# Kernel optimization log

Measured on AMD Instinct MI355X. Metric: run time of the kernel, lower is better.

## Reference

```python
import jax, jax.numpy as jnp
from jax import lax
import numpy as np

Bn, DM, HH, WW = 2, 192, 64, 64   # batch, d_model, H, W (H==W required by transpose-stack)
DI = 384   # d_inner = ssm_ratio * d_model
DS = 16    # ssm_d_state
ND = 4     # n_directions
CG = 12    # c_group
LN_EPS = 1e-5


def setup_inputs() -> dict:
    key = jax.random.key(0)
    k = jax.random.split(key, 16)
    w = lambda i, shape: jax.random.normal(k[i], shape, jnp.float32) * 0.05
    return {
        "x": jax.random.normal(k[0], (Bn, DM, HH, WW), jnp.float32),
        "in_proj_w": w(1, (DI, DM)),
        "dwconv_w": w(2, (DI, 1, 3, 3)),
        "dwconv_b": w(3, (DI,)),
        "x_down_w": w(4, (DS, DI)),
        "w_up_w": w(5, (CG * DI, DS)),
        "l_up_w": w(6, (ND * DI, DS)),
        "u_up_w": w(7, (ND * DI, DS)),
        "d_up_w": w(8, (ND * DI, DS)),
        "m_w": w(9, (ND,)),
        "grn_gamma": w(10, (DI,)),
        "grn_beta": w(11, (DI,)),
        "norm_w": 1.0 + w(12, (DI,)),
        "norm_b": w(13, (DI,)),
        "out_proj_w": w(14, (DM, DI)),
    }


def _conv1x1(w, x):
    return jnp.einsum('oc,bchw->bohw', w, x)


def _gate_recurrent(X, B, G1, G2, G3):
    # H[:, :, h, w] = B*X + G1*H[h-1,w-1] + G2*H[h,w-1] + G3*H[h+1,w-1]
    # sequential over width; vectorized over batch/channel/height via a column scan.
    def step(hprev, col):  # hprev: [B, C, H]
        xw, bw, g1w, g2w, g3w = col
        z = jnp.zeros_like(hprev[:, :, :1])
        up = jnp.concatenate([z, hprev[:, :, :-1]], axis=2)   # H[h-1, w-1]
        dn = jnp.concatenate([hprev[:, :, 1:], z], axis=2)    # H[h+1, w-1]
        h = bw * xw + g1w * up + g2w * hprev + g3w * dn
        return h, h

    cols = tuple(jnp.moveaxis(t, 3, 0) for t in (X, B, G1, G2, G3))  # [W, B, C, H]
    h0 = jnp.zeros(X.shape[:3], X.dtype)
    _, ys = lax.scan(step, h0, cols)
    return jnp.moveaxis(ys, 0, 3)  # [B, C, H, W]


def _normalize_w(Gl, Gm, Gr):
    gl, gm, gr = jax.nn.sigmoid(Gl), jax.nn.sigmoid(Gm), jax.nn.sigmoid(Gr)
    s = gl + gm + gr
    s = s.at[:, :, 0, :].set(gm[:, :, 0, :] + gr[:, :, 0, :])
    s = s.at[:, :, -1, :].set(gl[:, :, -1, :] + gm[:, :, -1, :])
    s = jnp.maximum(s, 1e-7)
    return gl / s, gm / s, gr / s


def reference(x, in_proj_w, dwconv_w, dwconv_b, x_down_w, w_up_w, l_up_w, u_up_w,
              d_up_w, m_w, grn_gamma, grn_beta, norm_w, norm_b, out_proj_w):
    Bsz = x.shape[0]
    # in_proj (1x1, no bias) + SiLU + depthwise 3x3 conv
    h = jax.nn.silu(_conv1x1(in_proj_w, x))
    h = lax.conv_general_dilated(h, dwconv_w, (1, 1), ((1, 1), (1, 1)),
                                 feature_group_count=DI) + dwconv_b[None, :, None, None]
    # forward_corev1
    xp = _conv1x1(x_down_w, h)            # [B, DS, H, W]
    ws = _conv1x1(w_up_w, xp)             # [B, 12*DI, H, W]
    Ls = _conv1x1(l_up_w, xp)             # [B, 4*DI, H, W]
    Us = _conv1x1(u_up_w, xp)
    Ds = _conv1x1(d_up_w, xp)
    hT = jnp.swapaxes(h, 2, 3)            # requires H==W
    xs = jnp.concatenate([h, hT, h[..., ::-1], hT[..., ::-1]], axis=1)  # [B, 4*DI, H, W]
    G1, G2, G3 = jnp.split(ws, 3, axis=1)
    g1, g2, g3 = _normalize_w(G1, G2, G3)
    out = _gate_recurrent(xs, Ls, g1, g2, g3)
    out = out * Us + xs * Ds
    # merge directions: view [B, 4, DI*H, W], 1x1 conv 4->1
    out = out.reshape(Bsz, ND, DI * HH, WW)
    y = jnp.einsum('d,bdxw->bxw', m_w, out).reshape(Bsz, DI, HH, WW)
    # LayerNorm2d over channel dim
    mu = y.mean(axis=1, keepdims=True)
    var = ((y - mu) ** 2).mean(axis=1, keepdims=True)
    y = (y - mu) * lax.rsqrt(var + LN_EPS) * norm_w[None, :, None, None] + norm_b[None, :, None, None]
    # GRN
    Gx = jnp.sqrt(jnp.sum(y * y, axis=(2, 3), keepdims=True))        # [B, C, 1, 1]
    Nx = Gx / (Gx.mean(axis=1, keepdims=True) + 1e-6)
    y = grn_gamma[None, :, None, None] * (y * Nx) + grn_beta[None, :, None, None] + y
    # out_proj (1x1, no bias)
    return _conv1x1(out_proj_w, y)
```

## Files before the change

### kernel.cpp

```cpp
#include <hip/hip_runtime.h>
#include <math.h>

#define Bn 2
#define DM 192
#define DI 384
#define DS 16
#define HH 64
#define WW 64
#define HW 4096
#define ND 4

__device__ __forceinline__ float sigmoidf_(float x) {
    return 1.0f / (1.0f + __expf(-x));
}

__global__ __launch_bounds__(256) void k_inproj(const float* __restrict__ x,
                                                const float* __restrict__ w,
                                                float* __restrict__ hpre) {
    int og = blockIdx.y, b = blockIdx.z;
    int p = blockIdx.x * 256 + threadIdx.x;
    const float* wr = w + (size_t)og * 16 * DM;
    const float* xb = x + (size_t)b * DM * HW + p;
    float acc[16];
#pragma unroll
    for (int j = 0; j < 16; ++j) acc[j] = 0.f;
    for (int c = 0; c < DM; c += 4) {
        float x0 = xb[(size_t)(c + 0) * HW];
        float x1 = xb[(size_t)(c + 1) * HW];
        float x2 = xb[(size_t)(c + 2) * HW];
        float x3 = xb[(size_t)(c + 3) * HW];
#pragma unroll
        for (int j = 0; j < 16; ++j) {
            const float* wj = wr + j * DM + c;
            acc[j] = fmaf(wj[0], x0, fmaf(wj[1], x1, fmaf(wj[2], x2, fmaf(wj[3], x3, acc[j]))));
        }
    }
    float* hb = hpre + (size_t)b * DI * HW + (size_t)(og * 16) * HW + p;
#pragma unroll
    for (int j = 0; j < 16; ++j) {
        float v = acc[j];
        hb[(size_t)j * HW] = v * (1.0f / (1.0f + __expf(-v)));
    }
}

__global__ __launch_bounds__(256) void k_dwconv(const float* __restrict__ hpre,
                                                const float* __restrict__ w,
                                                const float* __restrict__ bias,
                                                float* __restrict__ h) {
    int c = blockIdx.y, b = blockIdx.z;
    int p = blockIdx.x * 256 + threadIdx.x;
    int i = p >> 6, j = p & 63;
    const float* wp = w + c * 9;
    const float* src = hpre + ((size_t)b * DI + c) * HW;
    float acc = bias[c];
#pragma unroll
    for (int di = -1; di <= 1; ++di) {
        int ii = i + di;
        if (ii < 0 || ii >= HH) continue;
#pragma unroll
        for (int dj = -1; dj <= 1; ++dj) {
            int jj = j + dj;
            if (jj < 0 || jj >= WW) continue;
            acc = fmaf(wp[(di + 1) * 3 + (dj + 1)], src[ii * WW + jj], acc);
        }
    }
    h[((size_t)b * DI + c) * HW + p] = acc;
}

__global__ __launch_bounds__(256) void k_xdown(const float* __restrict__ h,
                                               const float* __restrict__ w,
                                               float* __restrict__ xpt) {
    int sq = blockIdx.y;
    int t = blockIdx.x * 256 + threadIdx.x;
    int b = t >> 12, p = t & 4095;
    const float* hb = h + (size_t)b * DI * HW + p;
    const float* w0 = w + (size_t)(4 * sq + 0) * DI;
    const float* w1 = w + (size_t)(4 * sq + 1) * DI;
    const float* w2 = w + (size_t)(4 * sq + 2) * DI;
    const float* w3 = w + (size_t)(4 * sq + 3) * DI;
    float a0 = 0.f, a1 = 0.f, a2 = 0.f, a3 = 0.f;
#pragma unroll 16
    for (int c = 0; c < DI; ++c) {
        float hv = hb[(size_t)c * HW];
        a0 = fmaf(w0[c], hv, a0);
        a1 = fmaf(w1[c], hv, a1);
        a2 = fmaf(w2[c], hv, a2);
        a3 = fmaf(w3[c], hv, a3);
    }
    float4 r = {a0, a1, a2, a3};
    *reinterpret_cast<float4*>(xpt + (size_t)t * 16 + 4 * sq) = r;
}

__global__ __launch_bounds__(256) void k_scan(const float* __restrict__ h,
                                              const float* __restrict__ xpt,
                                              const float* __restrict__ wup,
                                              const float* __restrict__ lup,
                                              const float* __restrict__ uup,
                                              const float* __restrict__ dup,
                                              const float* __restrict__ mw,
                                              float* __restrict__ y) {
    int c = blockIdx.x, b = blockIdx.y;
    int tid = threadIdx.x;
    int d = tid >> 6, hl = tid & 63;

    __shared__ float htile[64][65];
    __shared__ float acc[64][65];

    const float* hb = h + ((size_t)b * DI + c) * HW;
    for (int i = tid; i < HW; i += 256) {
        htile[i >> 6][i & 63] = hb[i];
        acc[i >> 6][i & 63] = 0.f;
    }

    int row = d * DI + c;
    const float* p1 = wup + (size_t)row * DS;
    const float* p2 = wup + (size_t)(4 * DI + row) * DS;
    const float* p3 = wup + (size_t)(8 * DI + row) * DS;
    const float* pL = lup + (size_t)row * DS;
    const float* pU = uup + (size_t)row * DS;
    const float* pD = dup + (size_t)row * DS;
    float w1[16], w2[16], w3[16], wL[16], wU[16], wD[16];
#pragma unroll
    for (int s = 0; s < 16; ++s) {
        w1[s] = p1[s]; w2[s] = p2[s]; w3[s] = p3[s];
        wL[s] = pL[s]; wU[s] = pU[s]; wD[s] = pD[s];
    }
    float md = mw[d];

    const float4* xq = reinterpret_cast<const float4*>(
        xpt + ((size_t)b * HW + (size_t)hl * 64) * DS);

    float4 c0 = xq[0], c1 = xq[1], c2 = xq[2], c3 = xq[3];
    float hprev = 0.f;
    __syncthreads();

    for (int w = 0; w < 64; ++w) {
        int nw = (w < 63) ? w + 1 : w;
        float4 n0 = xq[nw * 4 + 0], n1 = xq[nw * 4 + 1];
        float4 n2 = xq[nw * 4 + 2], n3 = xq[nw * 4 + 3];

        float xv[16] = {c0.x, c0.y, c0.z, c0.w, c1.x, c1.y, c1.z, c1.w,
                        c2.x, c2.y, c2.z, c2.w, c3.x, c3.y, c3.z, c3.w};
        float g1 = 0, g2 = 0, g3 = 0, L = 0, U = 0, Dv = 0;
#pragma unroll
        for (int s = 0; s < 16; ++s) {
            g1 = fmaf(w1[s], xv[s], g1);
            g2 = fmaf(w2[s], xv[s], g2);
            g3 = fmaf(w3[s], xv[s], g3);
            L  = fmaf(wL[s], xv[s], L);
            U  = fmaf(wU[s], xv[s], U);
            Dv = fmaf(wD[s], xv[s], Dv);
        }
        g1 = sigmoidf_(g1); g2 = sigmoidf_(g2); g3 = sigmoidf_(g3);
        float ssum = (hl == 0) ? (g2 + g3) : (hl == 63) ? (g1 + g2) : (g1 + g2 + g3);
        ssum = fmaxf(ssum, 1e-7f);
        float inv = 1.0f / ssum;
        float n1g = g1 * inv, n2g = g2 * inv, n3g = g3 * inv;

        float X;
        if (d == 0)      X = htile[hl][w];
        else if (d == 1) X = htile[w][hl];
        else if (d == 2) X = htile[hl][63 - w];
        else             X = htile[63 - w][hl];

        float up = __shfl_up(hprev, 1);
        float dn = __shfl_down(hprev, 1);
        if (hl == 0) up = 0.f;
        if (hl == 63) dn = 0.f;

        float hnew = fmaf(L, X, fmaf(n1g, up, fmaf(n2g, hprev, n3g * dn)));
        hprev = hnew;
        atomicAdd(&acc[hl][w], md * fmaf(hnew, U, X * Dv));

        c0 = n0; c1 = n1; c2 = n2; c3 = n3;
    }
    __syncthreads();
    float* yb = y + ((size_t)b * DI + c) * HW;
    for (int i = tid; i < HW; i += 256) yb[i] = acc[i >> 6][i & 63];
}

__global__ __launch_bounds__(256) void k_ln(float* __restrict__ y,
                                            const float* __restrict__ nw,
                                            const float* __restrict__ nb) {
    int lpx = threadIdx.x & 31, chunk = threadIdx.x >> 5;
    int gp = blockIdx.x * 32 + lpx;
    int b = gp >> 12, p = gp & 4095;
    float* yb = y + (size_t)b * DI * HW + p;

    float vv[48];
    float s = 0.f, s2 = 0.f;
#pragma unroll
    for (int ci = 0; ci < 48; ++ci) {
        float v = yb[(size_t)(chunk * 48 + ci) * HW];
        vv[ci] = v;
        s += v;
        s2 = fmaf(v, v, s2);
    }
    __shared__ float S[8][32], S2[8][32];
    S[chunk][lpx] = s;
    S2[chunk][lpx] = s2;
    __syncthreads();
    float ts = 0.f, ts2 = 0.f;
#pragma unroll
    for (int k = 0; k < 8; ++k) { ts += S[k][lpx]; ts2 += S2[k][lpx]; }
    float mu = ts * (1.0f / DI);
    float var = ts2 * (1.0f / DI) - mu * mu;
    float inv = rsqrtf(var + 1e-5f);
#pragma unroll
    for (int ci = 0; ci < 48; ++ci) {
        int c = chunk * 48 + ci;
        float v = (vv[ci] - mu) * inv;
        yb[(size_t)c * HW] = fmaf(v, nw[c], nb[c]);
    }
}

__global__ __launch_bounds__(256) void k_grnsum(const float* __restrict__ y,
                                                float* __restrict__ gx) {
    int c = blockIdx.x, b = blockIdx.y;
    const float* yb = y + ((size_t)b * DI + c) * HW;
    float s = 0.f;
#pragma unroll 4
    for (int i = threadIdx.x; i < HW; i += 256) {
        float v = yb[i];
        s = fmaf(v, v, s);
    }
#pragma unroll
    for (int o = 32; o > 0; o >>= 1) s += __shfl_down(s, o);
    __shared__ float red[4];
    int wid = threadIdx.x >> 6;
    if ((threadIdx.x & 63) == 0) red[wid] = s;
    __syncthreads();
    if (threadIdx.x == 0) gx[b * DI + c] = sqrtf(red[0] + red[1] + red[2] + red[3]);
}

__global__ __launch_bounds__(256) void k_grnscale(const float* __restrict__ gx,
                                                  const float* __restrict__ gamma,
                                                  float* __restrict__ sc) {
    int b = blockIdx.x;
    const float* g = gx + b * DI;
    float s = 0.f;
    for (int c = threadIdx.x; c < DI; c += 256) s += g[c];
#pragma unroll
    for (int o = 32; o > 0; o >>= 1) s += __shfl_down(s, o);
    __shared__ float red[4];
    __shared__ float meanv;
    int wid = threadIdx.x >> 6;
    if ((threadIdx.x & 63) == 0) red[wid] = s;
    __syncthreads();
    if (threadIdx.x == 0) meanv = (red[0] + red[1] + red[2] + red[3]) * (1.0f / DI);
    __syncthreads();
    float m = meanv;
    for (int c = threadIdx.x; c < DI; c += 256)
        sc[b * DI + c] = 1.0f + gamma[c] * (g[c] / (m + 1e-6f));
}

__global__ __launch_bounds__(256) void k_outproj(const float* __restrict__ y,
                                                 const float* __restrict__ w,
                                                 const float* __restrict__ sc_all,
                                                 const float* __restrict__ beta,
                                                 float* __restrict__ out) {
    int og = blockIdx.y, b = blockIdx.z;
    int p = blockIdx.x * 256 + threadIdx.x;
    const float* wr = w + (size_t)og * 8 * DI;
    const float* scb = sc_all + b * DI;
    const float* yb = y + (size_t)b * DI * HW + p;
    float acc[8];
#pragma unroll
    for (int j = 0; j < 8; ++j) acc[j] = 0.f;
    for (int c = 0; c < DI; c += 4) {
        float v0 = fmaf(yb[(size_t)(c + 0) * HW], scb[c + 0], beta[c + 0]);
        float v1 = fmaf(yb[(size_t)(c + 1) * HW], scb[c + 1], beta[c + 1]);
        float v2 = fmaf(yb[(size_t)(c + 2) * HW], scb[c + 2], beta[c + 2]);
        float v3 = fmaf(yb[(size_t)(c + 3) * HW], scb[c + 3], beta[c + 3]);
#pragma unroll
        for (int j = 0; j < 8; ++j) {
            const float* wj = wr + j * DI + c;
            acc[j] = fmaf(wj[0], v0, fmaf(wj[1], v1, fmaf(wj[2], v2, fmaf(wj[3], v3, acc[j]))));
        }
    }
    float* ob = out + (size_t)b * DM * HW + (size_t)(og * 8) * HW + p;
#pragma unroll
    for (int j = 0; j < 8; ++j) ob[(size_t)j * HW] = acc[j];
}

extern "C" void kernel_launch(void* const* d_in, const int* in_sizes, int n_in,
                              void* d_out, int out_size, void* d_ws, size_t ws_size,
                              hipStream_t stream) {
    (void)in_sizes; (void)n_in; (void)out_size; (void)ws_size;
    const float* x          = (const float*)d_in[0];
    const float* in_proj_w  = (const float*)d_in[1];
    const float* dwconv_w   = (const float*)d_in[2];
    const float* dwconv_b   = (const float*)d_in[3];
    const float* x_down_w   = (const float*)d_in[4];
    const float* w_up_w     = (const float*)d_in[5];
    const float* l_up_w     = (const float*)d_in[6];
    const float* u_up_w     = (const float*)d_in[7];
    const float* d_up_w     = (const float*)d_in[8];
    const float* m_w        = (const float*)d_in[9];
    const float* grn_gamma  = (const float*)d_in[10];
    const float* grn_beta   = (const float*)d_in[11];
    const float* norm_w     = (const float*)d_in[12];
    const float* norm_b     = (const float*)d_in[13];
    const float* out_proj_w = (const float*)d_in[14];

    float* ws = (float*)d_ws;
    const size_t NBIG = (size_t)Bn * DI * HW;
    float* hpre = ws;
    float* hbuf = ws + NBIG;
    float* xpt  = ws + 2 * NBIG;
    float* gx   = ws + 2 * NBIG + (size_t)Bn * HW * DS;
    float* sc   = gx + Bn * DI;
    float* y    = hpre;

    k_inproj<<<dim3(16, 24, 2), 256, 0, stream>>>(x, in_proj_w, hpre);
    k_dwconv<<<dim3(16, DI, Bn), 256, 0, stream>>>(hpre, dwconv_w, dwconv_b, hbuf);
    k_xdown<<<dim3(32, 4), 256, 0, stream>>>(hbuf, x_down_w, xpt);
    k_scan<<<dim3(DI, Bn), 256, 0, stream>>>(hbuf, xpt, w_up_w, l_up_w, u_up_w,
                                             d_up_w, m_w, y);
    k_ln<<<dim3(256), 256, 0, stream>>>(y, norm_w, norm_b);
    k_grnsum<<<dim3(DI, Bn), 256, 0, stream>>>(y, gx);
    k_grnscale<<<dim3(Bn), 256, 0, stream>>>(gx, grn_gamma, sc);
    k_outproj<<<dim3(16, 24, 2), 256, 0, stream>>>(y, out_proj_w, sc, grn_beta,
                                                   (float*)d_out);
}
```

Before: 227.2 us.

## Fuse GRN sum into LayerNorm, restructure xdown, streamline scan inner loop

The GRN sum-of-squares reduction moves into the LayerNorm kernel using wave shuffles and atomics, which removes a separate full pass over y. A memset is added to zero the accumulator. The x_down projection is rewritten so each block computes all 16 outputs for 64 pixels, splitting channels across waves and reducing through shared memory; this reads h once instead of four times. The scan loop precomputes the per-direction LDS pointer, folds m_w into the U/D weights, uses ds_bpermute and fast reciprocals, and double-buffers the xpt loads. Fast rcp slightly changes numerics, and the atomic float accumulation makes results order-dependent.

Result: slower. 289.8 us (+27.6%).

```diff
diff --git a/kernel.cpp b/kernel.cpp
--- a/kernel.cpp
+++ b/kernel.cpp
@@ -10,8 +10,9 @@
 #define HW 4096
 #define ND 4
 
-__device__ __forceinline__ float sigmoidf_(float x) {
-    return 1.0f / (1.0f + __expf(-x));
+__device__ __forceinline__ float fastrcp(float x) { return __builtin_amdgcn_rcpf(x); }
+__device__ __forceinline__ float fsig(float x) {
+    return fastrcp(1.0f + __expf(-x));
 }
 
 __global__ __launch_bounds__(256) void k_inproj(const float* __restrict__ x,
@@ -39,7 +40,7 @@
 #pragma unroll
     for (int j = 0; j < 16; ++j) {
         float v = acc[j];
-        hb[(size_t)j * HW] = v * (1.0f / (1.0f + __expf(-v)));
+        hb[(size_t)j * HW] = v * fastrcp(1.0f + __expf(-v));
     }
 }
 
@@ -70,25 +71,39 @@
 __global__ __launch_bounds__(256) void k_xdown(const float* __restrict__ h,
                                                const float* __restrict__ w,
                                                float* __restrict__ xpt) {
-    int sq = blockIdx.y;
-    int t = blockIdx.x * 256 + threadIdx.x;
-    int b = t >> 12, p = t & 4095;
+    __shared__ float red[4][64][17];
+    int tid = threadIdx.x;
+    int px = tid & 63, cw = tid >> 6;
+    int gp = blockIdx.x * 64 + px;
+    int b = gp >> 12, p = gp & 4095;
     const float* hb = h + (size_t)b * DI * HW + p;
-    const float* w0 = w + (size_t)(4 * sq + 0) * DI;
-    const float* w1 = w + (size_t)(4 * sq + 1) * DI;
-    const float* w2 = w + (size_t)(4 * sq + 2) * DI;
-    const float* w3 = w + (size_t)(4 * sq + 3) * DI;
-    float a0 = 0.f, a1 = 0.f, a2 = 0.f, a3 = 0.f;
-#pragma unroll 16
-    for (int c = 0; c < DI; ++c) {
-        float hv = hb[(size_t)c * HW];
-        a0 = fmaf(w0[c], hv, a0);
-        a1 = fmaf(w1[c], hv, a1);
-        a2 = fmaf(w2[c], hv, a2);
-        a3 = fmaf(w3[c], hv, a3);
-    }
-    float4 r = {a0, a1, a2, a3};
-    *reinterpret_cast<float4*>(xpt + (size_t)t * 16 + 4 * sq) = r;
+    int c0 = cw * 96;
+    float a[16];
+#pragma unroll
+    for (int s = 0; s < 16; ++s) a[s] = 0.f;
+    for (int cc = 0; cc < 96; cc += 4) {
+        float h0 = hb[(size_t)(c0 + cc + 0) * HW];
+        float h1 = hb[(size_t)(c0 + cc + 1) * HW];
+        float h2 = hb[(size_t)(c0 + cc + 2) * HW];
+        float h3 = hb[(size_t)(c0 + cc + 3) * HW];
+#pragma unroll
+        for (int s = 0; s < 16; ++s) {
+            const float* ws = w + (size_t)s * DI + c0 + cc;
+            a[s] = fmaf(ws[0], h0, fmaf(ws[1], h1, fmaf(ws[2], h2, fmaf(ws[3], h3, a[s]))));
+        }
+    }
+#pragma unroll
+    for (int s = 0; s < 16; ++s) red[cw][px][s] = a[s];
+    __syncthreads();
+    int sg = tid >> 6;
+    float4 r;
+    float* o = &r.x;
+#pragma unroll
+    for (int j = 0; j < 4; ++j) {
+        int s = sg * 4 + j;
+        o[j] = red[0][px][s] + red[1][px][s] + red[2][px][s] + red[3][px][s];
+    }
+    *reinterpret_cast<float4*>(xpt + (size_t)gp * 16 + sg * 4) = r;
 }
 
 __global__ __launch_bounds__(256) void k_scan(const float* __restrict__ h,
@@ -119,28 +134,38 @@
     const float* pL = lup + (size_t)row * DS;
     const float* pU = uup + (size_t)row * DS;
     const float* pD = dup + (size_t)row * DS;
+    float md = mw[d];
     float w1[16], w2[16], w3[16], wL[16], wU[16], wD[16];
 #pragma unroll
     for (int s = 0; s < 16; ++s) {
         w1[s] = p1[s]; w2[s] = p2[s]; w3[s] = p3[s];
-        wL[s] = pL[s]; wU[s] = pU[s]; wD[s] = pD[s];
-    }
-    float md = mw[d];
+        wL[s] = pL[s]; wU[s] = md * pU[s]; wD[s] = md * pD[s];
+    }
+
+    int xstep = (d & 1) ? 65 : 1;
+    int xbase = (d & 1) ? hl : hl * 65;
+    if (d & 2) { xbase += xstep * 63; xstep = -xstep; }
+    const float* xptr = &htile[0][0] + xbase;
+
+    int upA = ((hl - 1) & 63) << 2;
+    int dnA = ((hl + 1) & 63) << 2;
+    bool isTop = (hl == 0), isBot = (hl == 63);
+
+    float* accp = &acc[hl][0];
 
     const float4* xq = reinterpret_cast<const float4*>(
         xpt + ((size_t)b * HW + (size_t)hl * 64) * DS);
 
-    float4 c0 = xq[0], c1 = xq[1], c2 = xq[2], c3 = xq[3];
     float hprev = 0.f;
-    __syncthreads();
-
-    for (int w = 0; w < 64; ++w) {
-        int nw = (w < 63) ? w + 1 : w;
-        float4 n0 = xq[nw * 4 + 0], n1 = xq[nw * 4 + 1];
-        float4 n2 = xq[nw * 4 + 2], n3 = xq[nw * 4 + 3];
-
-        float xv[16] = {c0.x, c0.y, c0.z, c0.w, c1.x, c1.y, c1.z, c1.w,
-                        c2.x, c2.y, c2.z, c2.w, c3.x, c3.y, c3.z, c3.w};
+
+    float4 A0 = xq[0], A1 = xq[1], A2 = xq[2], A3 = xq[3];
+    float4 B0, B1, B2, B3;
+
+    __syncthreads();
+
+    auto docol = [&](const float4& q0, const float4& q1, const float4& q2, const float4& q3) {
+        float xv[16] = {q0.x, q0.y, q0.z, q0.w, q1.x, q1.y, q1.z, q1.w,
+                        q2.x, q2.y, q2.z, q2.w, q3.x, q3.y, q3.z, q3.w};
         float g1 = 0, g2 = 0, g3 = 0, L = 0, U = 0, Dv = 0;
 #pragma unroll
         for (int s = 0; s < 16; ++s) {
@@ -151,29 +176,30 @@
             U  = fmaf(wU[s], xv[s], U);
             Dv = fmaf(wD[s], xv[s], Dv);
         }
-        g1 = sigmoidf_(g1); g2 = sigmoidf_(g2); g3 = sigmoidf_(g3);
-        float ssum = (hl == 0) ? (g2 + g3) : (hl == 63) ? (g1 + g2) : (g1 + g2 + g3);
-        ssum = fmaxf(ssum, 1e-7f);
-        float inv = 1.0f / ssum;
-        float n1g = g1 * inv, n2g = g2 * inv, n3g = g3 * inv;
-
-        float X;
-        if (d == 0)      X = htile[hl][w];
-        else if (d == 1) X = htile[w][hl];
-        else if (d == 2) X = htile[hl][63 - w];
-        else             X = htile[63 - w][hl];
-
-        float up = __shfl_up(hprev, 1);
-        float dn = __shfl_down(hprev, 1);
-        if (hl == 0) up = 0.f;
-        if (hl == 63) dn = 0.f;
-
-        float hnew = fmaf(L, X, fmaf(n1g, up, fmaf(n2g, hprev, n3g * dn)));
+        g1 = fsig(g1); g2 = fsig(g2); g3 = fsig(g3);
+        float ssum = g2 + (isTop ? 0.f : g1) + (isBot ? 0.f : g3);
+        float inv = fastrcp(fmaxf(ssum, 1e-7f));
+        float X = *xptr; xptr += xstep;
+        float up = __int_as_float(__builtin_amdgcn_ds_bpermute(upA, __float_as_int(hprev)));
+        float dn = __int_as_float(__builtin_amdgcn_ds_bpermute(dnA, __float_as_int(hprev)));
+        up = isTop ? 0.f : up;
+        dn = isBot ? 0.f : dn;
+        float hnew = fmaf(L, X, inv * fmaf(g1, up, fmaf(g2, hprev, g3 * dn)));
         hprev = hnew;
-        atomicAdd(&acc[hl][w], md * fmaf(hnew, U, X * Dv));
-
-        c0 = n0; c1 = n1; c2 = n2; c3 = n3;
-    }
+        atomicAdd(accp, fmaf(hnew, U, X * Dv));
+        accp += 1;
+    };
+
+    for (int w = 0; w < 64; w += 2) {
+        const float4* pn = xq + (w + 1) * 4;
+        B0 = pn[0]; B1 = pn[1]; B2 = pn[2]; B3 = pn[3];
+        docol(A0, A1, A2, A3);
+        int w2i = (w + 2 < 64) ? w + 2 : 63;
+        const float4* pm = xq + w2i * 4;
+        A0 = pm[0]; A1 = pm[1]; A2 = pm[2]; A3 = pm[3];
+        docol(B0, B1, B2, B3);
+    }
+
     __syncthreads();
     float* yb = y + ((size_t)b * DI + c) * HW;
     for (int i = tid; i < HW; i += 256) yb[i] = acc[i >> 6][i & 63];
@@ -181,7 +207,8 @@
 
 __global__ __launch_bounds__(256) void k_ln(float* __restrict__ y,
                                             const float* __restrict__ nw,
-                                            const float* __restrict__ nb) {
+                                            const float* __restrict__ nb,
+                                            float* __restrict__ gxsum) {
     int lpx = threadIdx.x & 31, chunk = threadIdx.x >> 5;
     int gp = blockIdx.x * 32 + lpx;
     int b = gp >> 12, p = gp & 4095;
@@ -210,36 +237,27 @@
     for (int ci = 0; ci < 48; ++ci) {
         int c = chunk * 48 + ci;
         float v = (vv[ci] - mu) * inv;
-        yb[(size_t)c * HW] = fmaf(v, nw[c], nb[c]);
-    }
-}
-
-__global__ __launch_bounds__(256) void k_grnsum(const float* __restrict__ y,
-                                                float* __restrict__ gx) {
-    int c = blockIdx.x, b = blockIdx.y;
-    const float* yb = y + ((size_t)b * DI + c) * HW;
-    float s = 0.f;
-#pragma unroll 4
-    for (int i = threadIdx.x; i < HW; i += 256) {
-        float v = yb[i];
-        s = fmaf(v, v, s);
-    }
-#pragma unroll
-    for (int o = 32; o > 0; o >>= 1) s += __shfl_down(s, o);
-    __shared__ float red[4];
-    int wid = threadIdx.x >> 6;
-    if ((threadIdx.x & 63) == 0) red[wid] = s;
-    __syncthreads();
-    if (threadIdx.x == 0) gx[b * DI + c] = sqrtf(red[0] + red[1] + red[2] + red[3]);
-}
-
-__global__ __launch_bounds__(256) void k_grnscale(const float* __restrict__ gx,
+        float o = fmaf(v, nw[c], nb[c]);
+        yb[(size_t)c * HW] = o;
+        float r = o * o;
+        r += __shfl_xor(r, 16);
+        r += __shfl_xor(r, 8);
+        r += __shfl_xor(r, 4);
+        r += __shfl_xor(r, 2);
+        r += __shfl_xor(r, 1);
+        if (lpx == 0) atomicAdd(&gxsum[b * DI + c], r);
+    }
+}
+
+__global__ __launch_bounds__(256) void k_grnscale(const float* __restrict__ gxsum,
                                                   const float* __restrict__ gamma,
                                                   float* __restrict__ sc) {
     int b = blockIdx.x;
-    const float* g = gx + b * DI;
-    float s = 0.f;
-    for (int c = threadIdx.x; c < DI; c += 256) s += g[c];
+    const float* g = gxsum + b * DI;
+    int cidx = threadIdx.x;
+    float gx0 = sqrtf(g[cidx]);
+    float gx1 = (cidx < DI - 256) ? sqrtf(g[cidx + 256]) : 0.f;
+    float s = gx0 + gx1;
 #pragma unroll
     for (int o = 32; o > 0; o >>= 1) s += __shfl_down(s, o);
     __shared__ float red[4];
@@ -249,9 +267,10 @@
     __syncthreads();
     if (threadIdx.x == 0) meanv = (red[0] + red[1] + red[2] + red[3]) * (1.0f / DI);
     __syncthreads();
-    float m = meanv;
-    for (int c = threadIdx.x; c < DI; c += 256)
-        sc[b * DI + c] = 1.0f + gamma[c] * (g[c] / (m + 1e-6f));
+    float m = meanv + 1e-6f;
+    sc[b * DI + cidx] = 1.0f + gamma[cidx] * (gx0 / m);
+    if (cidx < DI - 256)
+        sc[b * DI + cidx + 256] = 1.0f + gamma[cidx + 256] * (gx1 / m);
 }
 
 __global__ __launch_bounds__(256) void k_outproj(const float* __restrict__ y,
@@ -314,11 +333,11 @@
 
     k_inproj<<<dim3(16, 24, 2), 256, 0, stream>>>(x, in_proj_w, hpre);
     k_dwconv<<<dim3(16, DI, Bn), 256, 0, stream>>>(hpre, dwconv_w, dwconv_b, hbuf);
-    k_xdown<<<dim3(32, 4), 256, 0, stream>>>(hbuf, x_down_w, xpt);
+    k_xdown<<<dim3(128), 256, 0, stream>>>(hbuf, x_down_w, xpt);
     k_scan<<<dim3(DI, Bn), 256, 0, stream>>>(hbuf, xpt, w_up_w, l_up_w, u_up_w,
                                              d_up_w, m_w, y);
-    k_ln<<<dim3(256), 256, 0, stream>>>(y, norm_w, norm_b);
-    k_grnsum<<<dim3(DI, Bn), 256, 0, stream>>>(y, gx);
+    hipMemsetAsync(gx, 0, Bn * DI * sizeof(float), stream);
+    k_ln<<<dim3(256), 256, 0, stream>>>(y, norm_w, norm_b, gx);
     k_grnscale<<<dim3(Bn), 256, 0, stream>>>(gx, grn_gamma, sc);
     k_outproj<<<dim3(16, 24, 2), 256, 0, stream>>>(y, out_proj_w, sc, grn_beta,
                                                    (float*)d_out);
```
